# Kernel tuning notes

Hardware: AMD Instinct MI355X
Metric: run time of the kernel (lower is better)

## Reference

```python
import jax, jax.numpy as jnp
import numpy as np

NEG_INF = jnp.float32(-jnp.inf)


def setup_inputs() -> dict:
    key = jax.random.key(0)
    k1, k2, k3, k4 = jax.random.split(key, 4)
    B, T, E = 8, 2048, 1024
    H_DK = 1024  # dk * num_heads
    scale = 1.0 / np.sqrt(E)
    x = jax.random.normal(k1, (B, T, E), dtype=jnp.float32)
    Wq = jax.random.normal(k2, (E, H_DK), dtype=jnp.float32) * scale
    Wk = jax.random.normal(k3, (E, H_DK), dtype=jnp.float32) * scale
    Wv = jax.random.normal(k4, (E, H_DK), dtype=jnp.float32) * scale
    return {"x": x, "Wq": Wq, "Wk": Wk, "Wv": Wv, "dk": 64}


def reference(x, Wq, Wk, Wv, dk):
    # x: [B, T, E]; Wq/Wk/Wv: [E, H*dk] (heads never split in original module)
    Q = jnp.einsum("bte,ed->btd", x, Wq)
    K = jnp.einsum("bte,ed->btd", x, Wk)
    V = jnp.einsum("bte,ed->btd", x, Wv)
    energy = jnp.einsum("bqd,bkd->bqk", Q, K)  # [B, T, T]
    B, T, _ = energy.shape
    # padding mask derived from first query row: lengths[b] = #nonzero of energy[b,0,:]
    lengths = jnp.sum(energy[:, 0] != 0, axis=-1)  # [B]
    j = jnp.arange(T)
    pad_mask = j[None, :] >= lengths[:, None]          # [B, T] -> key positions masked
    causal_mask = j[None, :] > j[:, None]              # [T, T]
    mask = pad_mask[:, None, :] | causal_mask[None, :, :]  # [B, T, T]
    energy = jnp.where(mask, NEG_INF, energy)
    score = jax.nn.softmax(energy / jnp.sqrt(jnp.float32(dk)), axis=-1)
    return jnp.einsum("bqk,bkd->bqd", score, V)
```

## Files before the change

### kernel.cpp

```cpp
#include <hip/hip_runtime.h>

#define DEV __device__ __forceinline__

using f32x4 = __attribute__((ext_vector_type(4))) float;
using f16x8 = __attribute__((ext_vector_type(8))) _Float16;
using f16x4 = __attribute__((ext_vector_type(4))) _Float16;

constexpr int Bc = 8, Tc = 2048, Ec = 1024, Hc = 1024;
constexpr int Mc = Bc * Tc;
constexpr int SLOT = 256 * 32;

DEV f32x4 mfma16(f16x8 a, f16x8 b, f32x4 c) {
    return __builtin_amdgcn_mfma_f32_16x16x32_f16(a, b, c, 0, 0, 0);
}
DEV unsigned short f16bits(float f) { return __builtin_bit_cast(unsigned short, (_Float16)f); }
DEV float f16val(unsigned short u) { return (float)__builtin_bit_cast(_Float16, u); }

DEV void gload16(const _Float16* g, _Float16* l) {
    __builtin_amdgcn_global_load_lds(
        (const __attribute__((address_space(1))) unsigned int*)g,
        (__attribute__((address_space(3))) unsigned int*)l, 16, 0, 0);
}

DEV int swz_off(int R, int lk) {
    return ((R >> 1) << 6) + ((((((R & 1) << 2) | lk) ^ ((R >> 1) & 7))) << 3);
}

__global__ __launch_bounds__(256) void prep_x(const float* __restrict__ x,
                                              _Float16* __restrict__ xf, int n) {
    int i = (blockIdx.x * 256 + threadIdx.x) * 4;
    if (i >= n) return;
    f32x4 v = *reinterpret_cast<const f32x4*>(x + i);
    f16x4 h;
#pragma unroll
    for (int j = 0; j < 4; j++) h[j] = (_Float16)v[j];
    *reinterpret_cast<f16x4*>(xf + i) = h;
}

__global__ __launch_bounds__(256) void prep_w(const float* __restrict__ wq,
                                              const float* __restrict__ wk,
                                              const float* __restrict__ wv,
                                              _Float16* __restrict__ wall) {
    __shared__ float tile[32][33];
    const int z = blockIdx.z;
    const float* src = (z == 0) ? wq : (z == 1) ? wk : wv;
    _Float16* dh = wall + (size_t)z * 1024 * Ec;
    const int n0 = blockIdx.x * 32, e0 = blockIdx.y * 32;
    const int tx = threadIdx.x & 31, ty = threadIdx.x >> 5;
#pragma unroll
    for (int j = 0; j < 32; j += 8)
        tile[ty + j][tx] = src[(size_t)(e0 + ty + j) * Hc + n0 + tx];
    __syncthreads();
#pragma unroll
    for (int j = 0; j < 32; j += 8)
        dh[(size_t)(n0 + ty + j) * Ec + e0 + tx] = (_Float16)tile[tx][ty + j];
}

template <int EPI>
DEV void gemm_body(int bx, int by, int z,
                   const _Float16* __restrict__ Ah, const _Float16* __restrict__ Bh,
                   void* __restrict__ out0, void* __restrict__ out2,
                   const int* __restrict__ dkp,
                   int lda, int ldb, size_t aBS, size_t bBS, size_t oBS, int nkt,
                   _Float16* sAb, _Float16* sBb) {
    if (EPI == 3) nkt = (by + 1) * 8;

    Ah += (size_t)z * aBS;
    Bh += (size_t)z * bBS;

    const float scale = (EPI == 2) ? (1.0f / sqrtf((float)*dkp)) : 1.0f;

    const int tid = threadIdx.x;
    const int wave = tid >> 6, lane = tid & 63;
    const int lr = lane & 15, lk = lane >> 4;
    const int wm = wave >> 2, wn = wave & 3;
    const int m0 = by * 256, n0 = bx * 256;

    const int so = (lane & 7) ^ (lane >> 3);
    const int strow = 2 * (lane >> 3) + (so >> 2);
    const int stcol = (so & 3) * 8;
    const size_t aoff0 = (size_t)(m0 + (wave * 2 + 0) * 16 + strow) * lda + stcol;
    const size_t aoff1 = (size_t)(m0 + (wave * 2 + 1) * 16 + strow) * lda + stcol;
    const size_t boff0 = (size_t)(n0 + (wave * 2 + 0) * 16 + strow) * ldb + stcol;
    const size_t boff1 = (size_t)(n0 + (wave * 2 + 1) * 16 + strow) * ldb + stcol;
    const int ld0 = (wave * 2 + 0) * 512, ld1 = (wave * 2 + 1) * 512;

    auto stage = [&](int sv, int slot) {
        const int kk = sv * 32;
        _Float16* dA = sAb + slot * SLOT;
        _Float16* dB = sBb + slot * SLOT;
        gload16(Ah + aoff0 + kk, dA + ld0);
        gload16(Ah + aoff1 + kk, dA + ld1);
        gload16(Bh + boff0 + kk, dB + ld0);
        gload16(Bh + boff1 + kk, dB + ld1);
    };

    f32x4 acc[8][4] = {};

    stage(0, 0);
    stage(1, 1);
    asm volatile("s_waitcnt vmcnt(4)" ::: "memory");
    __builtin_amdgcn_s_barrier();

    int rP = 0;
    for (int P = 0; P < nkt; ++P) {
        const _Float16* cA = sAb + rP * SLOT;
        const _Float16* cB = sBb + rP * SLOT;
        f16x8 af[8], bfr[4];

#pragma unroll
        for (int nj = 0; nj < 4; nj++)
            bfr[nj] = *reinterpret_cast<const f16x8*>(
                &cB[swz_off(wn * 64 + nj * 16 + lr, lk)]);
#pragma unroll
        for (int mi = 0; mi < 8; mi++)
            af[mi] = *reinterpret_cast<const f16x8*>(
                &cA[swz_off(wm * 128 + mi * 16 + lr, lk)]);

        int rs = rP + 2; if (rs >= 3) rs -= 3;
        if (P + 2 < nkt) stage(P + 2, rs);

        __builtin_amdgcn_s_setprio(1);
#pragma unroll
        for (int mi = 0; mi < 8; mi++)
#pragma unroll
            for (int nj = 0; nj < 4; nj++)
                acc[mi][nj] = mfma16(af[mi], bfr[nj], acc[mi][nj]);
        __builtin_amdgcn_s_setprio(0);

        if (P + 2 < nkt) {
            asm volatile("s_waitcnt vmcnt(4)" ::: "memory");
            __builtin_amdgcn_s_barrier();
        } else if (P + 1 < nkt) {
            asm volatile("s_waitcnt vmcnt(0)" ::: "memory");
            __builtin_amdgcn_s_barrier();
        }
        if (++rP == 3) rP = 0;
    }

#pragma unroll
    for (int mi = 0; mi < 8; mi++)
#pragma unroll
        for (int nj = 0; nj < 4; nj++) {
            const int gn = n0 + wn * 64 + nj * 16 + lr;
            if (EPI == 1) {
                const int gm0 = m0 + wm * 128 + mi * 16 + lk * 4;
                const int bb = gm0 >> 11, t = gm0 & (Tc - 1);
                f16x4 pk;
#pragma unroll
                for (int r = 0; r < 4; r++) pk[r] = (_Float16)acc[mi][nj][r];
                *reinterpret_cast<f16x4*>(
                    &((_Float16*)out0)[((size_t)(bb * Hc + gn)) * Tc + t]) = pk;
            } else if (EPI == 0) {
                _Float16* od = (gn < 1024) ? (_Float16*)out0 : (_Float16*)out2;
                const int cc = gn & 1023;
#pragma unroll
                for (int r = 0; r < 4; r++) {
                    const int gm = m0 + wm * 128 + mi * 16 + lk * 4 + r;
                    od[(size_t)gm * Hc + cc] = (_Float16)acc[mi][nj][r];
                }
            } else {
#pragma unroll
                for (int r = 0; r < 4; r++) {
                    const int gm = m0 + wm * 128 + mi * 16 + lk * 4 + r;
                    const float v = acc[mi][nj][r];
                    if (EPI == 2) {
                        const float e = (gn > gm) ? -INFINITY : v * scale;
                        ((unsigned short*)out0)[(size_t)z * oBS + (size_t)gm * Tc + gn] =
                            f16bits(e);
                    } else {
                        ((float*)out0)[(size_t)z * oBS + (size_t)gm * Hc + gn] = v;
                    }
                }
            }
        }
}

__global__ __launch_bounds__(512, 2) void k_qkv(
        const _Float16* __restrict__ Xf, const _Float16* __restrict__ Wall,
        _Float16* __restrict__ Qf, _Float16* __restrict__ Kf,
        _Float16* __restrict__ Vt, const int* __restrict__ dkp) {
    __shared__ _Float16 sA[3][SLOT];
    __shared__ _Float16 sB[3][SLOT];
    const int i = blockIdx.x;
    if (i < 512) {
        const int w = (i & 7) * 64 + (i >> 3);
        const int by = w >> 3, bx = w & 7;
        gemm_body<0>(bx, by, 0, Xf, Wall, Qf, Kf, dkp,
                     Ec, Ec, 0, 0, 0, 32, sA[0], sB[0]);
    } else {
        const int j = i - 512;
        gemm_body<1>(j & 3, j >> 2, 0, Xf, Wall + (size_t)2048 * Ec,
                     Vt, nullptr, dkp, Ec, Ec, 0, 0, 0, 32, sA[0], sB[0]);
    }
}

__global__ __launch_bounds__(512, 2) void k_energy(
        const _Float16* __restrict__ Qf, const _Float16* __restrict__ Kf,
        unsigned short* __restrict__ S, const int* __restrict__ dkp) {
    __shared__ _Float16 sA[3][SLOT];
    __shared__ _Float16 sB[3][SLOT];
    const int i = blockIdx.x;
    const int b = i / 36;
    int t = i - b * 36;
    int by = 0;
    while (t >= by + 1) { t -= by + 1; by++; }
    gemm_body<2>(t, by, b, Qf, Kf, S, nullptr, dkp,
                 Hc, Hc, (size_t)Tc * Hc, (size_t)Tc * Hc, (size_t)Tc * Tc, 32,
                 sA[0], sB[0]);
}

__global__ __launch_bounds__(512, 2) void k_pv(
        const _Float16* __restrict__ S, const _Float16* __restrict__ Vt,
        float* __restrict__ out, const int* __restrict__ dkp) {
    __shared__ _Float16 sA[3][SLOT];
    __shared__ _Float16 sB[3][SLOT];
    gemm_body<3>(blockIdx.x, blockIdx.y, blockIdx.z, S, Vt, out, nullptr, dkp,
                 Tc, Tc, (size_t)Tc * Tc, (size_t)Hc * Tc, (size_t)Tc * Hc, 0,
                 sA[0], sB[0]);
}

__global__ __launch_bounds__(256) void softmax_k(unsigned short* __restrict__ S) {
    const int q = blockIdx.x & (Tc - 1);
    const int b = blockIdx.x >> 11;
    const int tid = threadIdx.x;
    const int c0 = tid * 8;
    const int limit = ((q >> 8) + 1) << 8;
    const bool active = c0 < limit;
    unsigned short* row = S + ((size_t)b * Tc + q) * Tc;

    float v[8];
    if (active) {
        uint4 raw = *reinterpret_cast<const uint4*>(row + c0);
        unsigned u[4] = {raw.x, raw.y, raw.z, raw.w};
#pragma unroll
        for (int p = 0; p < 4; p++) {
            v[2 * p]     = f16val((unsigned short)(u[p] & 0xFFFFu));
            v[2 * p + 1] = f16val((unsigned short)(u[p] >> 16));
        }
#pragma unroll
        for (int i = 0; i < 8; i++)
            if (c0 + i > q) v[i] = -INFINITY;
    } else {
#pragma unroll
        for (int i = 0; i < 8; i++) v[i] = -INFINITY;
    }

    float m = v[0];
#pragma unroll
    for (int i = 1; i < 8; i++) m = fmaxf(m, v[i]);
#pragma unroll
    for (int off = 1; off < 64; off <<= 1) m = fmaxf(m, __shfl_xor(m, off));
    __shared__ float red[4];
    if ((tid & 63) == 0) red[tid >> 6] = m;
    __syncthreads();
    m = fmaxf(fmaxf(red[0], red[1]), fmaxf(red[2], red[3]));

    float e[8], s = 0.f;
#pragma unroll
    for (int i = 0; i < 8; i++) {
        e[i] = __expf(v[i] - m);
        s += e[i];
    }
#pragma unroll
    for (int off = 1; off < 64; off <<= 1) s += __shfl_xor(s, off);
    __syncthreads();
    if ((tid & 63) == 0) red[tid >> 6] = s;
    __syncthreads();
    s = red[0] + red[1] + red[2] + red[3];
    const float inv = 1.0f / s;

    if (active) {
        unsigned o[4];
#pragma unroll
        for (int p = 0; p < 4; p++) {
            unsigned short a = f16bits(e[2 * p] * inv);
            unsigned short bb = f16bits(e[2 * p + 1] * inv);
            o[p] = (unsigned)a | ((unsigned)bb << 16);
        }
        uint4 w; w.x = o[0]; w.y = o[1]; w.z = o[2]; w.w = o[3];
        *reinterpret_cast<uint4*>(row + c0) = w;
    }
}

extern "C" void kernel_launch(void* const* d_in, const int* in_sizes, int n_in,
                              void* d_out, int out_size, void* d_ws, size_t ws_size,
                              hipStream_t stream) {
    const float* x  = (const float*)d_in[0];
    const float* Wq = (const float*)d_in[1];
    const float* Wk = (const float*)d_in[2];
    const float* Wv = (const float*)d_in[3];
    const int*   dk = (const int*)d_in[4];
    float* out = (float*)d_out;
    char* ws = (char*)d_ws;

    const size_t SZ_XE = (size_t)Mc * Ec * 2;
    const size_t SZ_W  = (size_t)Ec * Hc * 2;

    size_t o = 0;
    auto nxt = [&](size_t bytes) { void* p = ws + o; o += bytes; return p; };
    _Float16* Qf   = (_Float16*)nxt(SZ_XE);
    _Float16* Kf   = (_Float16*)nxt(SZ_XE);
    _Float16* Vt   = (_Float16*)nxt(SZ_XE);
    _Float16* Xf   = (_Float16*)nxt(SZ_XE);
    _Float16* Wall = (_Float16*)nxt(3 * SZ_W);
    unsigned short* S = (unsigned short*)Xf;
    (void)ws_size; (void)in_sizes; (void)n_in; (void)out_size;

    prep_x<<<(Mc * Ec / 4 + 255) / 256, 256, 0, stream>>>(x, Xf, Mc * Ec);
    prep_w<<<dim3(32, 32, 3), 256, 0, stream>>>(Wq, Wk, Wv, Wall);

    k_qkv<<<768, 512, 0, stream>>>(Xf, Wall, Qf, Kf, Vt, dk);

    k_energy<<<288, 512, 0, stream>>>(Qf, Kf, (unsigned short*)S, dk);

    softmax_k<<<Bc * Tc, 256, 0, stream>>>((unsigned short*)S);

    k_pv<<<dim3(4, 8, Bc), 512, 0, stream>>>((const _Float16*)S, Vt, out, dk);
}
```

Baseline: 287.3 us.

## Shrink GEMM block tile to 128x256 with 4 waves and reorder PV blocks

Changes the shared GEMM body from 256x256 tiles with 8 waves to 128x256 tiles with 4 waves, each wave now covering all 128 rows and a 64-column slice. B-tile staging grows to 4 loads per wave, and the vmcnt waits are adjusted to match. Grids double for the QKV, energy and PV kernels, and the causal triangle enumeration is redone at 128-row granularity. PV blocks are paired light/heavy (qb and 15-qb) to balance the causal work. The aim is finer causal granularity and better load balance, at the cost of less B reuse per block and more global traffic for B.

```diff
diff --git a/kernel.cpp b/kernel.cpp
--- a/kernel.cpp
+++ b/kernel.cpp
@@ -8,7 +8,8 @@
 
 constexpr int Bc = 8, Tc = 2048, Ec = 1024, Hc = 1024;
 constexpr int Mc = Bc * Tc;
-constexpr int SLOT = 256 * 32;
+constexpr int SLOTA = 128 * 32;
+constexpr int SLOTB = 256 * 32;
 
 DEV f32x4 mfma16(f16x8 a, f16x8 b, f32x4 c) {
     return __builtin_amdgcn_mfma_f32_16x16x32_f16(a, b, c, 0, 0, 0);
@@ -57,13 +58,13 @@
 }
 
 template <int EPI>
-DEV void gemm_body(int bx, int by, int z,
+DEV void gemm_body(int bx, int mt, int z,
                    const _Float16* __restrict__ Ah, const _Float16* __restrict__ Bh,
                    void* __restrict__ out0, void* __restrict__ out2,
                    const int* __restrict__ dkp,
                    int lda, int ldb, size_t aBS, size_t bBS, size_t oBS, int nkt,
                    _Float16* sAb, _Float16* sBb) {
-    if (EPI == 3) nkt = (by + 1) * 8;
+    if (EPI == 3) nkt = ((mt >> 1) + 1) * 8;
 
     Ah += (size_t)z * aBS;
     Bh += (size_t)z * bBS;
@@ -73,39 +74,42 @@
     const int tid = threadIdx.x;
     const int wave = tid >> 6, lane = tid & 63;
     const int lr = lane & 15, lk = lane >> 4;
-    const int wm = wave >> 2, wn = wave & 3;
-    const int m0 = by * 256, n0 = bx * 256;
+    const int wn = wave;
+    const int m0 = mt * 128, n0 = bx * 256;
 
     const int so = (lane & 7) ^ (lane >> 3);
     const int strow = 2 * (lane >> 3) + (so >> 2);
     const int stcol = (so & 3) * 8;
     const size_t aoff0 = (size_t)(m0 + (wave * 2 + 0) * 16 + strow) * lda + stcol;
     const size_t aoff1 = (size_t)(m0 + (wave * 2 + 1) * 16 + strow) * lda + stcol;
-    const size_t boff0 = (size_t)(n0 + (wave * 2 + 0) * 16 + strow) * ldb + stcol;
-    const size_t boff1 = (size_t)(n0 + (wave * 2 + 1) * 16 + strow) * ldb + stcol;
-    const int ld0 = (wave * 2 + 0) * 512, ld1 = (wave * 2 + 1) * 512;
+    size_t boff[4];
+#pragma unroll
+    for (int l = 0; l < 4; l++)
+        boff[l] = (size_t)(n0 + (wave * 4 + l) * 16 + strow) * ldb + stcol;
+    const int lda0 = (wave * 2 + 0) * 512, lda1 = (wave * 2 + 1) * 512;
 
     auto stage = [&](int sv, int slot) {
         const int kk = sv * 32;
-        _Float16* dA = sAb + slot * SLOT;
-        _Float16* dB = sBb + slot * SLOT;
-        gload16(Ah + aoff0 + kk, dA + ld0);
-        gload16(Ah + aoff1 + kk, dA + ld1);
-        gload16(Bh + boff0 + kk, dB + ld0);
-        gload16(Bh + boff1 + kk, dB + ld1);
+        _Float16* dA = sAb + slot * SLOTA;
+        _Float16* dB = sBb + slot * SLOTB;
+        gload16(Ah + aoff0 + kk, dA + lda0);
+        gload16(Ah + aoff1 + kk, dA + lda1);
+#pragma unroll
+        for (int l = 0; l < 4; l++)
+            gload16(Bh + boff[l] + kk, dB + (wave * 4 + l) * 512);
     };
 
     f32x4 acc[8][4] = {};
 
     stage(0, 0);
     stage(1, 1);
-    asm volatile("s_waitcnt vmcnt(4)" ::: "memory");
+    asm volatile("s_waitcnt vmcnt(6)" ::: "memory");
     __builtin_amdgcn_s_barrier();
 
     int rP = 0;
     for (int P = 0; P < nkt; ++P) {
-        const _Float16* cA = sAb + rP * SLOT;
-        const _Float16* cB = sBb + rP * SLOT;
+        const _Float16* cA = sAb + rP * SLOTA;
+        const _Float16* cB = sBb + rP * SLOTB;
         f16x8 af[8], bfr[4];
 
 #pragma unroll
@@ -115,7 +119,7 @@
 #pragma unroll
         for (int mi = 0; mi < 8; mi++)
             af[mi] = *reinterpret_cast<const f16x8*>(
-                &cA[swz_off(wm * 128 + mi * 16 + lr, lk)]);
+                &cA[swz_off(mi * 16 + lr, lk)]);
 
         int rs = rP + 2; if (rs >= 3) rs -= 3;
         if (P + 2 < nkt) stage(P + 2, rs);
@@ -129,7 +133,7 @@
         __builtin_amdgcn_s_setprio(0);
 
         if (P + 2 < nkt) {
-            asm volatile("s_waitcnt vmcnt(4)" ::: "memory");
+            asm volatile("s_waitcnt vmcnt(6)" ::: "memory");
             __builtin_amdgcn_s_barrier();
         } else if (P + 1 < nkt) {
             asm volatile("s_waitcnt vmcnt(0)" ::: "memory");
@@ -144,7 +148,7 @@
         for (int nj = 0; nj < 4; nj++) {
             const int gn = n0 + wn * 64 + nj * 16 + lr;
             if (EPI == 1) {
-                const int gm0 = m0 + wm * 128 + mi * 16 + lk * 4;
+                const int gm0 = m0 + mi * 16 + lk * 4;
                 const int bb = gm0 >> 11, t = gm0 & (Tc - 1);
                 f16x4 pk;
 #pragma unroll
@@ -156,13 +160,13 @@
                 const int cc = gn & 1023;
 #pragma unroll
                 for (int r = 0; r < 4; r++) {
-                    const int gm = m0 + wm * 128 + mi * 16 + lk * 4 + r;
+                    const int gm = m0 + mi * 16 + lk * 4 + r;
                     od[(size_t)gm * Hc + cc] = (_Float16)acc[mi][nj][r];
                 }
             } else {
 #pragma unroll
                 for (int r = 0; r < 4; r++) {
-                    const int gm = m0 + wm * 128 + mi * 16 + lk * 4 + r;
+                    const int gm = m0 + mi * 16 + lk * 4 + r;
                     const float v = acc[mi][nj][r];
                     if (EPI == 2) {
                         const float e = (gn > gm) ? -INFINITY : v * scale;
@@ -176,46 +180,51 @@
         }
 }
 
-__global__ __launch_bounds__(512, 2) void k_qkv(
+__global__ __launch_bounds__(256, 2) void k_qkv(
         const _Float16* __restrict__ Xf, const _Float16* __restrict__ Wall,
         _Float16* __restrict__ Qf, _Float16* __restrict__ Kf,
         _Float16* __restrict__ Vt, const int* __restrict__ dkp) {
-    __shared__ _Float16 sA[3][SLOT];
-    __shared__ _Float16 sB[3][SLOT];
+    __shared__ _Float16 sA[3][SLOTA];
+    __shared__ _Float16 sB[3][SLOTB];
     const int i = blockIdx.x;
-    if (i < 512) {
-        const int w = (i & 7) * 64 + (i >> 3);
-        const int by = w >> 3, bx = w & 7;
-        gemm_body<0>(bx, by, 0, Xf, Wall, Qf, Kf, dkp,
+    if (i < 1024) {
+        const int w = (i & 7) * 128 + (i >> 3);
+        const int mt = w >> 3, bx = w & 7;
+        gemm_body<0>(bx, mt, 0, Xf, Wall, Qf, Kf, dkp,
                      Ec, Ec, 0, 0, 0, 32, sA[0], sB[0]);
     } else {
-        const int j = i - 512;
+        const int j = i - 1024;
         gemm_body<1>(j & 3, j >> 2, 0, Xf, Wall + (size_t)2048 * Ec,
                      Vt, nullptr, dkp, Ec, Ec, 0, 0, 0, 32, sA[0], sB[0]);
     }
 }
 
-__global__ __launch_bounds__(512, 2) void k_energy(
+__global__ __launch_bounds__(256, 2) void k_energy(
         const _Float16* __restrict__ Qf, const _Float16* __restrict__ Kf,
         unsigned short* __restrict__ S, const int* __restrict__ dkp) {
-    __shared__ _Float16 sA[3][SLOT];
-    __shared__ _Float16 sB[3][SLOT];
+    __shared__ _Float16 sA[3][SLOTA];
+    __shared__ _Float16 sB[3][SLOTB];
     const int i = blockIdx.x;
-    const int b = i / 36;
-    int t = i - b * 36;
-    int by = 0;
-    while (t >= by + 1) { t -= by + 1; by++; }
-    gemm_body<2>(t, by, b, Qf, Kf, S, nullptr, dkp,
+    const int b = i / 72;
+    int t = i - b * 72;
+    int qb = 0;
+    while (t >= (qb >> 1) + 1) { t -= (qb >> 1) + 1; qb++; }
+    gemm_body<2>(t, qb, b, Qf, Kf, S, nullptr, dkp,
                  Hc, Hc, (size_t)Tc * Hc, (size_t)Tc * Hc, (size_t)Tc * Tc, 32,
                  sA[0], sB[0]);
 }
 
-__global__ __launch_bounds__(512, 2) void k_pv(
+__global__ __launch_bounds__(256, 2) void k_pv(
         const _Float16* __restrict__ S, const _Float16* __restrict__ Vt,
         float* __restrict__ out, const int* __restrict__ dkp) {
-    __shared__ _Float16 sA[3][SLOT];
-    __shared__ _Float16 sB[3][SLOT];
-    gemm_body<3>(blockIdx.x, blockIdx.y, blockIdx.z, S, Vt, out, nullptr, dkp,
+    __shared__ _Float16 sA[3][SLOTA];
+    __shared__ _Float16 sB[3][SLOTB];
+    const int lin = blockIdx.x;
+    const int b = lin >> 6;
+    const int r = lin & 63;
+    const int bx = r & 3, half = (r >> 2) & 1, pp = r >> 3;
+    const int qb = half ? 15 - pp : pp;
+    gemm_body<3>(bx, qb, b, S, Vt, out, nullptr, dkp,
                  Tc, Tc, (size_t)Tc * Tc, (size_t)Hc * Tc, (size_t)Tc * Hc, 0,
                  sA[0], sB[0]);
 }
@@ -310,11 +319,11 @@
     prep_x<<<(Mc * Ec / 4 + 255) / 256, 256, 0, stream>>>(x, Xf, Mc * Ec);
     prep_w<<<dim3(32, 32, 3), 256, 0, stream>>>(Wq, Wk, Wv, Wall);
 
-    k_qkv<<<768, 512, 0, stream>>>(Xf, Wall, Qf, Kf, Vt, dk);
-
-    k_energy<<<288, 512, 0, stream>>>(Qf, Kf, (unsigned short*)S, dk);
+    k_qkv<<<1536, 256, 0, stream>>>(Xf, Wall, Qf, Kf, Vt, dk);
+
+    k_energy<<<576, 256, 0, stream>>>(Qf, Kf, (unsigned short*)S, dk);
 
     softmax_k<<<Bc * Tc, 256, 0, stream>>>((unsigned short*)S);
 
-    k_pv<<<dim3(4, 8, Bc), 512, 0, stream>>>((const _Float16*)S, Vt, out, dk);
-}
+    k_pv<<<512, 256, 0, stream>>>((const _Float16*)S, Vt, out, dk);
+}
```

After: 295.0 us. +2.7%, slower.

## Use 4 waves per GEMM block with 128x128 per-wave tiles

Applied to the files above, without the earlier changes.

The shared GEMM body now runs with 256 threads (4 waves) per 256x256 block instead of 8 waves. Each wave computes a 128x128 sub-tile (8x8 MFMA accumulators) and issues 4 A plus 4 B async LDS loads per stage, with the wait counts adjusted to match. This raises MFMA work per LDS fragment load and cuts the wave count sharing each barrier. In exchange it needs far more accumulator registers (256 floats per lane), lowers occupancy to one block per CU, and leaves fewer waves to hide load latency.

```diff
diff --git a/kernel.cpp b/kernel.cpp
--- a/kernel.cpp
+++ b/kernel.cpp
@@ -57,13 +57,13 @@
 }
 
 template <int EPI>
-DEV void gemm_body(int bx, int by, int z,
+DEV void gemm_body(int bx, int mt, int z,
                    const _Float16* __restrict__ Ah, const _Float16* __restrict__ Bh,
                    void* __restrict__ out0, void* __restrict__ out2,
                    const int* __restrict__ dkp,
                    int lda, int ldb, size_t aBS, size_t bBS, size_t oBS, int nkt,
                    _Float16* sAb, _Float16* sBb) {
-    if (EPI == 3) nkt = (by + 1) * 8;
+    if (EPI == 3) nkt = (mt + 1) * 8;
 
     Ah += (size_t)z * aBS;
     Bh += (size_t)z * bBS;
@@ -73,45 +73,47 @@
     const int tid = threadIdx.x;
     const int wave = tid >> 6, lane = tid & 63;
     const int lr = lane & 15, lk = lane >> 4;
-    const int wm = wave >> 2, wn = wave & 3;
-    const int m0 = by * 256, n0 = bx * 256;
+    const int wm = wave >> 1, wn2 = wave & 1;
+    const int m0 = mt * 256, n0 = bx * 256;
 
     const int so = (lane & 7) ^ (lane >> 3);
     const int strow = 2 * (lane >> 3) + (so >> 2);
     const int stcol = (so & 3) * 8;
-    const size_t aoff0 = (size_t)(m0 + (wave * 2 + 0) * 16 + strow) * lda + stcol;
-    const size_t aoff1 = (size_t)(m0 + (wave * 2 + 1) * 16 + strow) * lda + stcol;
-    const size_t boff0 = (size_t)(n0 + (wave * 2 + 0) * 16 + strow) * ldb + stcol;
-    const size_t boff1 = (size_t)(n0 + (wave * 2 + 1) * 16 + strow) * ldb + stcol;
-    const int ld0 = (wave * 2 + 0) * 512, ld1 = (wave * 2 + 1) * 512;
+    size_t aoff[4], boff[4];
+#pragma unroll
+    for (int l = 0; l < 4; l++) {
+        aoff[l] = (size_t)(m0 + (wave * 4 + l) * 16 + strow) * lda + stcol;
+        boff[l] = (size_t)(n0 + (wave * 4 + l) * 16 + strow) * ldb + stcol;
+    }
 
     auto stage = [&](int sv, int slot) {
         const int kk = sv * 32;
         _Float16* dA = sAb + slot * SLOT;
         _Float16* dB = sBb + slot * SLOT;
-        gload16(Ah + aoff0 + kk, dA + ld0);
-        gload16(Ah + aoff1 + kk, dA + ld1);
-        gload16(Bh + boff0 + kk, dB + ld0);
-        gload16(Bh + boff1 + kk, dB + ld1);
+#pragma unroll
+        for (int l = 0; l < 4; l++) {
+            gload16(Ah + aoff[l] + kk, dA + (wave * 4 + l) * 512);
+            gload16(Bh + boff[l] + kk, dB + (wave * 4 + l) * 512);
+        }
     };
 
-    f32x4 acc[8][4] = {};
+    f32x4 acc[8][8] = {};
 
     stage(0, 0);
     stage(1, 1);
-    asm volatile("s_waitcnt vmcnt(4)" ::: "memory");
+    asm volatile("s_waitcnt vmcnt(8)" ::: "memory");
     __builtin_amdgcn_s_barrier();
 
     int rP = 0;
     for (int P = 0; P < nkt; ++P) {
         const _Float16* cA = sAb + rP * SLOT;
         const _Float16* cB = sBb + rP * SLOT;
-        f16x8 af[8], bfr[4];
-
-#pragma unroll
-        for (int nj = 0; nj < 4; nj++)
+        f16x8 af[8], bfr[8];
+
+#pragma unroll
+        for (int nj = 0; nj < 8; nj++)
             bfr[nj] = *reinterpret_cast<const f16x8*>(
-                &cB[swz_off(wn * 64 + nj * 16 + lr, lk)]);
+                &cB[swz_off(wn2 * 128 + nj * 16 + lr, lk)]);
 #pragma unroll
         for (int mi = 0; mi < 8; mi++)
             af[mi] = *reinterpret_cast<const f16x8*>(
@@ -124,12 +126,12 @@
 #pragma unroll
         for (int mi = 0; mi < 8; mi++)
 #pragma unroll
-            for (int nj = 0; nj < 4; nj++)
+            for (int nj = 0; nj < 8; nj++)
                 acc[mi][nj] = mfma16(af[mi], bfr[nj], acc[mi][nj]);
         __builtin_amdgcn_s_setprio(0);
 
         if (P + 2 < nkt) {
-            asm volatile("s_waitcnt vmcnt(4)" ::: "memory");
+            asm volatile("s_waitcnt vmcnt(8)" ::: "memory");
             __builtin_amdgcn_s_barrier();
         } else if (P + 1 < nkt) {
             asm volatile("s_waitcnt vmcnt(0)" ::: "memory");
@@ -141,8 +143,8 @@
 #pragma unroll
     for (int mi = 0; mi < 8; mi++)
 #pragma unroll
-        for (int nj = 0; nj < 4; nj++) {
-            const int gn = n0 + wn * 64 + nj * 16 + lr;
+        for (int nj = 0; nj < 8; nj++) {
+            const int gn = n0 + wn2 * 128 + nj * 16 + lr;
             if (EPI == 1) {
                 const int gm0 = m0 + wm * 128 + mi * 16 + lk * 4;
                 const int bb = gm0 >> 11, t = gm0 & (Tc - 1);
@@ -176,7 +178,7 @@
         }
 }
 
-__global__ __launch_bounds__(512, 2) void k_qkv(
+__global__ __launch_bounds__(256, 1) void k_qkv(
         const _Float16* __restrict__ Xf, const _Float16* __restrict__ Wall,
         _Float16* __restrict__ Qf, _Float16* __restrict__ Kf,
         _Float16* __restrict__ Vt, const int* __restrict__ dkp) {
@@ -195,7 +197,7 @@
     }
 }
 
-__global__ __launch_bounds__(512, 2) void k_energy(
+__global__ __launch_bounds__(256, 1) void k_energy(
         const _Float16* __restrict__ Qf, const _Float16* __restrict__ Kf,
         unsigned short* __restrict__ S, const int* __restrict__ dkp) {
     __shared__ _Float16 sA[3][SLOT];
@@ -210,7 +212,7 @@
                  sA[0], sB[0]);
 }
 
-__global__ __launch_bounds__(512, 2) void k_pv(
+__global__ __launch_bounds__(256, 1) void k_pv(
         const _Float16* __restrict__ S, const _Float16* __restrict__ Vt,
         float* __restrict__ out, const int* __restrict__ dkp) {
     __shared__ _Float16 sA[3][SLOT];
@@ -310,11 +312,11 @@
     prep_x<<<(Mc * Ec / 4 + 255) / 256, 256, 0, stream>>>(x, Xf, Mc * Ec);
     prep_w<<<dim3(32, 32, 3), 256, 0, stream>>>(Wq, Wk, Wv, Wall);
 
-    k_qkv<<<768, 512, 0, stream>>>(Xf, Wall, Qf, Kf, Vt, dk);
-
-    k_energy<<<288, 512, 0, stream>>>(Qf, Kf, (unsigned short*)S, dk);
+    k_qkv<<<768, 256, 0, stream>>>(Xf, Wall, Qf, Kf, Vt, dk);
+
+    k_energy<<<288, 256, 0, stream>>>(Qf, Kf, (unsigned short*)S, dk);
 
     softmax_k<<<Bc * Tc, 256, 0, stream>>>((unsigned short*)S);
 
-    k_pv<<<dim3(4, 8, Bc), 512, 0, stream>>>((const _Float16*)S, Vt, out, dk);
-}
+    k_pv<<<dim3(4, 8, Bc), 256, 0, stream>>>((const _Float16*)S, Vt, out, dk);
+}
```

Result: slower. 300.0 us (+4.4%).
